# Kernel tuning notes

Measured on AMD Instinct MI355X. Metric: run time of the kernel, lower is better.

## Reference

```python
import jax, jax.numpy as jnp
import numpy as np
import math

# Model dims (see shape_source)
BATCH, SEQ, HH, WW = 32, 128, 32, 32   # x: (B, seq_len, H, W); L = H*W = 1024
D_MODEL = 1024                          # hidden_dim
N2 = 4                                  # n=8 -> 4 complex S4D modes
L_MAX = 64                              # SSM kernel length (l_max)


def _layernorm(x, gamma, beta, eps=1e-5):
    mu = jnp.mean(x, axis=-1, keepdims=True)
    var = jnp.var(x, axis=-1, keepdims=True)
    return (x - mu) * jax.lax.rsqrt(var + eps) * gamma + beta


def setup_inputs() -> dict:
    key = jax.random.key(0)
    ks = jax.random.split(key, 12)
    d_in = SEQ  # d_input = d_output = seq_len
    inp = {
        "x": jax.random.normal(ks[0], (BATCH, SEQ, HH, WW), dtype=jnp.float32),
        # encoder Linear(d_input -> d_model)
        "W_enc": jax.random.normal(ks[1], (d_in, D_MODEL), dtype=jnp.float32) / math.sqrt(d_in),
        "b_enc": jnp.zeros((D_MODEL,), dtype=jnp.float32),
        # S4D SSM parameters (per d_model channel, N2 complex modes)
        "log_dt": (jax.random.uniform(ks[2], (D_MODEL,), dtype=jnp.float32)
                   * (math.log(0.1) - math.log(0.001)) + math.log(0.001)),
        "A_log_real": jnp.full((D_MODEL, N2), math.log(0.5), dtype=jnp.float32),
        "A_imag": jnp.broadcast_to(math.pi * jnp.arange(N2, dtype=jnp.float32), (D_MODEL, N2)).copy(),
        "C_real": jax.random.normal(ks[3], (D_MODEL, N2), dtype=jnp.float32) * 0.5,
        "C_imag": jax.random.normal(ks[4], (D_MODEL, N2), dtype=jnp.float32) * 0.5,
        "D": jax.random.normal(ks[5], (D_MODEL,), dtype=jnp.float32),
        # position-wise GLU mixing Linear(d_model -> 2*d_model)
        "W_glu": jax.random.normal(ks[6], (D_MODEL, 2 * D_MODEL), dtype=jnp.float32) / math.sqrt(D_MODEL),
        "b_glu": jnp.zeros((2 * D_MODEL,), dtype=jnp.float32),
        "ln_gamma": jnp.ones((D_MODEL,), dtype=jnp.float32),
        "ln_beta": jnp.zeros((D_MODEL,), dtype=jnp.float32),
        # decoder Linear(d_model -> d_output)
        "W_dec": jax.random.normal(ks[7], (D_MODEL, d_in), dtype=jnp.float32) / math.sqrt(D_MODEL),
        "b_dec": jnp.zeros((d_in,), dtype=jnp.float32),
    }
    return inp


def reference(x, W_enc, b_enc, log_dt, A_log_real, A_imag, C_real, C_imag, D,
              W_glu, b_glu, ln_gamma, ln_beta, W_dec, b_dec):
    Bsz, S, Hh, Ww = x.shape
    L = Hh * Ww
    u = x.reshape(Bsz, S, L)                                  # (B, d_input, L)
    # encoder applied per position along L
    h = jnp.einsum('bdl,de->ble', u, W_enc) + b_enc           # (B, L, d_model)

    # ---- S4D kernel (ZOH discretization, B=1, diagonal A) ----
    dt = jnp.exp(log_dt)                                      # (d,)
    A = -jnp.exp(A_log_real) + 1j * A_imag                    # (d, n2) complex
    Cc = C_real + 1j * C_imag
    dtA = A * dt[:, None]                                     # (d, n2)
    Bd = (jnp.exp(dtA) - 1.0) / A                             # ZOH input matrix
    t = jnp.arange(L_MAX)
    vand = jnp.exp(dtA[:, :, None] * t)                       # (d, n2, l_max)
    K = 2.0 * jnp.einsum('dn,dnl->dl', Cc * Bd, vand).real    # (d, l_max)

    # ---- causal FFT convolution along L + skip D*u ----
    z = jnp.swapaxes(h, 1, 2)                                 # (B, d, L)
    n_fft = L + L_MAX
    y = jnp.fft.irfft(jnp.fft.rfft(z, n=n_fft) * jnp.fft.rfft(K, n=n_fft), n=n_fft)[..., :L]
    y = y + D[:, None] * z                                    # (B, d, L)

    # ---- block: GELU -> GLU mixing -> residual -> LayerNorm ----
    y = jax.nn.gelu(jnp.swapaxes(y, 1, 2))                    # (B, L, d)
    g = y @ W_glu + b_glu                                     # (B, L, 2d)
    g = g[..., :D_MODEL] * jax.nn.sigmoid(g[..., D_MODEL:])
    h = _layernorm(h + g, ln_gamma, ln_beta)                  # (B, L, d)

    out = h @ W_dec + b_dec                                   # (B, L, d_output)
    out = jnp.swapaxes(out, 1, 2).reshape(Bsz, S, Hh, Ww)
    return out
```

## Files before the change

kernel.cpp:

```cpp
#include <hip/hip_runtime.h>
#include <hip/hip_bf16.h>
#include <math.h>

#define B_ 32
#define S_ 128
#define L_ 1024
#define D_ 1024

typedef unsigned short u16;
typedef __attribute__((ext_vector_type(8))) __bf16 bf16x8;
typedef __attribute__((ext_vector_type(8))) short short8;
typedef __attribute__((ext_vector_type(4))) float f32x4;

__device__ __forceinline__ float bf2f(u16 u) {
    return __uint_as_float(((unsigned)u) << 16);
}
__device__ __forceinline__ u16 f2bf(float f) {
    unsigned u = __float_as_uint(f);
    u += 0x7FFF + ((u >> 16) & 1);
    return (u16)(u >> 16);
}
__device__ __forceinline__ float gelu_tanh(float x) {
    float x3 = x * x * x;
    float t = tanhf(0.7978845608028654f * (x + 0.044715f * x3));
    return 0.5f * x * (1.0f + t);
}
__device__ __forceinline__ float sigmoidf(float x) {
    return 1.0f / (1.0f + expf(-x));
}
__device__ __forceinline__ void gld16(const void* g, void* l) {
    __builtin_amdgcn_global_load_lds((const __attribute__((address_space(1))) void*)g,
                                     (__attribute__((address_space(3))) void*)l, 16, 0, 0);
}

__device__ __forceinline__ void tcast_body(
        const float* __restrict__ src, u16* __restrict__ dst, int R, int C,
        const float* __restrict__ rowscale, int bx, int by, int t,
        float (*tile)[65]) {
    int c0 = bx * 64, r0 = by * 64;
    #pragma unroll
    for (int p = 0; p < 4; ++p) {
        int fid = p * 256 + t;
        int rr = fid >> 4, cc = (fid & 15) * 4;
        float4 v = *(const float4*)&src[(size_t)(r0 + rr) * C + c0 + cc];
        float sc = rowscale ? rowscale[r0 + rr] : 1.0f;
        tile[rr][cc + 0] = v.x * sc; tile[rr][cc + 1] = v.y * sc;
        tile[rr][cc + 2] = v.z * sc; tile[rr][cc + 3] = v.w * sc;
    }
    __syncthreads();
    #pragma unroll
    for (int p = 0; p < 4; ++p) {
        int fid = p * 256 + t;
        int rr = fid >> 4, cc = (fid & 15) * 4;
        ushort4 o;
        o.x = f2bf(tile[cc + 0][rr]);
        o.y = f2bf(tile[cc + 1][rr]);
        o.z = f2bf(tile[cc + 2][rr]);
        o.w = f2bf(tile[cc + 3][rr]);
        *(ushort4*)&dst[(size_t)(c0 + rr) * R + r0 + cc] = o;
    }
}

__global__ __launch_bounds__(256) void k_prep(
        const float* __restrict__ Wg, u16* __restrict__ WgT,
        const float* __restrict__ Wd, const float* __restrict__ gam,
        u16* __restrict__ WdT,
        const float* __restrict__ We, u16* __restrict__ WeT,
        const float* __restrict__ x, u16* __restrict__ xb,
        const float* __restrict__ ldt, const float* __restrict__ Alr,
        const float* __restrict__ Aim, const float* __restrict__ Cr,
        const float* __restrict__ Ci, float* __restrict__ Kt,
        const float* __restrict__ bet, const float* __restrict__ bd,
        float* __restrict__ c12) {
    __shared__ float tile[64][65];
    __shared__ float r1[4], r2[4];
    int blk = blockIdx.x;
    int t = threadIdx.x;
    if (blk < 512) {
        tcast_body(Wg, WgT, 1024, 2048, nullptr, blk & 31, blk >> 5, t, tile);
    } else if (blk < 544) {
        int id = blk - 512;
        tcast_body(Wd, WdT, 1024, 128, gam, id & 1, id >> 1, t, tile);
    } else if (blk < 576) {
        int id = blk - 544;
        tcast_body(We, WeT, 128, 1024, nullptr, id & 15, id >> 4, t, tile);
    } else if (blk < 1600) {
        int id = blk - 576;
        int bz = id >> 5;
        tcast_body(x + (size_t)bz * 131072, xb + (size_t)bz * 131072,
                   128, 1024, nullptr, id & 15, (id >> 4) & 1, t, tile);
    } else if (blk < 1856) {
        int tid = (blk - 1600) * 256 + t;
        int d = tid & (D_ - 1);
        int j = tid >> 10;
        float dt = expf(ldt[d]);
        float acc = 0.f;
        #pragma unroll
        for (int n = 0; n < 4; ++n) {
            float ar = -expf(Alr[d * 4 + n]);
            float ai = Aim[d * 4 + n];
            float wr = ar * dt, wi = ai * dt;
            float ew = expf(wr);
            float sw, cw; sincosf(wi, &sw, &cw);
            float ur = ew * cw - 1.0f, ui = ew * sw;
            float inv = 1.0f / (ar * ar + ai * ai);
            float bdr = (ur * ar + ui * ai) * inv;
            float bdi = (ui * ar - ur * ai) * inv;
            float cr = Cr[d * 4 + n], ci = Ci[d * 4 + n];
            float cbr = cr * bdr - ci * bdi;
            float cbi = cr * bdi + ci * bdr;
            float ej = expf(wr * (float)j);
            float sj, cj; sincosf(wi * (float)j, &sj, &cj);
            acc += 2.0f * ej * (cbr * cj - cbi * sj);
        }
        Kt[j * D_ + d] = acc;
    } else {
        int s = blk - 1856;
        float a1 = 0.f, a2 = 0.f;
        #pragma unroll
        for (int it = 0; it < 4; ++it) {
            int k = it * 256 + t;
            float w = Wd[(size_t)k * 128 + s];
            a1 += gam[k] * w;
            a2 += bet[k] * w;
        }
        #pragma unroll
        for (int off = 32; off > 0; off >>= 1) {
            a1 += __shfl_down(a1, off);
            a2 += __shfl_down(a2, off);
        }
        int wid = t >> 6, lane = t & 63;
        if (lane == 0) { r1[wid] = a1; r2[wid] = a2; }
        __syncthreads();
        if (t == 0) {
            c12[s] = r1[0] + r1[1] + r1[2] + r1[3];
            c12[128 + s] = r2[0] + r2[1] + r2[2] + r2[3] + bd[s];
        }
    }
}

__global__ __launch_bounds__(256) void k_enc_mfma(
        const u16* __restrict__ xb, const u16* __restrict__ WeT,
        const float* __restrict__ be, u16* __restrict__ hb) {
    __shared__ u16 As[128 * 128];
    __shared__ u16 Bs[128 * 128];
    int t = threadIdx.x;
    int lane = t & 63, wid = t >> 6;
    int wr = wid & 1, wc = wid >> 1;
    int orig = blockIdx.x;
    int wgid = (orig & 7) * 256 + (orig >> 3);
    int m0 = (wgid >> 3) * 128;
    int e0 = (wgid & 7) * 128;

    #pragma unroll
    for (int c = 0; c < 8; ++c) {
        int ch = wid * 8 + c;
        int r = ch * 4 + (lane >> 4);
        int g = (lane & 15) ^ (r & 15);
        gld16(&xb[(size_t)(m0 + r) * 128 + g * 8], &As[ch * 512]);
        gld16(&WeT[(size_t)(e0 + r) * 128 + g * 8], &Bs[ch * 512]);
    }
    int co4[4];
    #pragma unroll
    for (int kh = 0; kh < 4; ++kh)
        co4[kh] = ((((lane >> 4) + kh * 4) ^ (lane & 15)) * 8);
    int arow[4], brow[4];
    #pragma unroll
    for (int i = 0; i < 4; ++i) arow[i] = (wr * 64 + i * 16 + (lane & 15)) * 128;
    #pragma unroll
    for (int q = 0; q < 4; ++q) brow[q] = (wc * 64 + q * 16 + (lane & 15)) * 128;

    __syncthreads();
    f32x4 acc[4][4] = {};
    #pragma unroll
    for (int kh = 0; kh < 4; ++kh) {
        bf16x8 af[4], bfr[4];
        #pragma unroll
        for (int i = 0; i < 4; ++i) af[i] = *(const bf16x8*)&As[arow[i] + co4[kh]];
        #pragma unroll
        for (int q = 0; q < 4; ++q) bfr[q] = *(const bf16x8*)&Bs[brow[q] + co4[kh]];
        __builtin_amdgcn_s_setprio(1);
        #pragma unroll
        for (int i = 0; i < 4; ++i)
            #pragma unroll
            for (int q = 0; q < 4; ++q)
                acc[i][q] = __builtin_amdgcn_mfma_f32_16x16x32_bf16(af[i], bfr[q], acc[i][q], 0, 0, 0);
        __builtin_amdgcn_s_setprio(0);
    }
    #pragma unroll
    for (int q = 0; q < 4; ++q) {
        int e = e0 + wc * 64 + q * 16 + (lane & 15);
        float bias = be[e];
        #pragma unroll
        for (int i = 0; i < 4; ++i) {
            #pragma unroll
            for (int r = 0; r < 4; ++r) {
                int m = m0 + wr * 64 + i * 16 + (lane >> 4) * 4 + r;
                hb[(size_t)m * 1024 + e] = f2bf(acc[i][q][r] + bias);
            }
        }
    }
}

__global__ __launch_bounds__(256) void k_conv(
        const u16* __restrict__ hb, const float* __restrict__ Kt,
        const float* __restrict__ Dv, u16* __restrict__ yg) {
    __shared__ float hs[128][68];
    int b = blockIdx.y;
    int d0 = blockIdx.x * 64;
    int t = threadIdx.x;
    int dl = t & 63, lg = t >> 6;
    {
        int r = 64 + (t >> 2), cg0 = (t & 3) * 16;
        #pragma unroll
        for (int j = 0; j < 4; ++j)
            *(float4*)&hs[r][cg0 + j * 4] = make_float4(0.f, 0.f, 0.f, 0.f);
    }
    float kr[64];
    #pragma unroll
    for (int j = 0; j < 64; ++j) kr[j] = Kt[j * 1024 + d0 + dl];
    float Dd = Dv[d0 + dl];
    int lr = t >> 2, cg = (t & 3) * 16;
    for (int it = 0; it < 16; ++it) {
        int l0 = it * 64;
        {
            int l = l0 + lr;
            int row = l & 127;
            const u16* src = &hb[((size_t)b * 1024 + l) * 1024 + d0 + cg];
            #pragma unroll
            for (int h = 0; h < 2; ++h) {
                ushort4 u0 = *(const ushort4*)&src[h * 8];
                ushort4 u1 = *(const ushort4*)&src[h * 8 + 4];
                *(float4*)&hs[row][cg + h * 8] =
                    make_float4(bf2f(u0.x), bf2f(u0.y), bf2f(u0.z), bf2f(u0.w));
                *(float4*)&hs[row][cg + h * 8 + 4] =
                    make_float4(bf2f(u1.x), bf2f(u1.y), bf2f(u1.z), bf2f(u1.w));
            }
        }
        __syncthreads();
        float acc[16] = {};
        int rb = l0 + 65 + lg * 16;
        #pragma unroll
        for (int s = 0; s < 15; ++s) {
            float hv = hs[(rb + s) & 127][dl];
            #pragma unroll
            for (int i = 0; i <= 14; ++i)
                if (i <= s) acc[i] = fmaf(kr[i + 63 - s], hv, acc[i]);
        }
        #pragma unroll
        for (int s = 15; s < 64; ++s) {
            float hv = hs[(rb + s) & 127][dl];
            #pragma unroll
            for (int i = 0; i < 16; ++i)
                acc[i] = fmaf(kr[i + 63 - s], hv, acc[i]);
        }
        #pragma unroll
        for (int s = 64; s < 79; ++s) {
            float hv = hs[(rb + s) & 127][dl];
            #pragma unroll
            for (int i = 1; i < 16; ++i)
                if (i >= s - 63) acc[i] = fmaf(kr[i + 63 - s], hv, acc[i]);
        }
        #pragma unroll
        for (int i = 0; i < 16; ++i) {
            int l = l0 + lg * 16 + i;
            float z = hs[l & 127][dl];
            float y = acc[i] + Dd * z;
            yg[((size_t)b * 1024 + l) * 1024 + d0 + dl] = f2bf(gelu_tanh(y));
        }
        __syncthreads();
    }
}

__global__ __launch_bounds__(512, 2) void k_glu256(
        const u16* __restrict__ yg, const u16* __restrict__ WgT,
        const float* __restrict__ bg, u16* __restrict__ hb) {
    __shared__ u16 S[65536];
    int t = threadIdx.x;
    int lane = t & 63, wid = t >> 6;
    int wr = wid >> 2, wc = wid & 3;

    int orig = blockIdx.x;
    int wgid = (orig & 7) * 128 + (orig >> 3);
    int m0 = (wgid >> 3) * 256;
    int p0g = (wgid & 7) * 128;

    int gofs = (((lane & 7) ^ ((lane >> 3) & 7)) * 8);
    int ch0 = wid * 2, ch1 = ch0 + 1;
    int dst0 = ch0 * 512 + lane * 8;
    int dst1 = ch1 * 512 + lane * 8;
    int gmA[2][2], gmB[2][2];
    #pragma unroll
    for (int h = 0; h < 2; ++h) {
        #pragma unroll
        for (int j = 0; j < 2; ++j) {
            int ch = ch0 + j;
            gmA[h][j] = m0 + (ch >> 3) * 128 + h * 64 + (ch & 7) * 8 + (lane >> 3);
            int r = (ch >> 2) * 64 + h * 32 + (ch & 3) * 8 + (lane >> 3);
            gmB[h][j] = ((r >> 4) & 1) * 1024 + p0g + (((r >> 5) << 4) | (r & 15));
        }
    }
    int co[2];
    co[0] = (((lane >> 4) + 0) ^ (lane & 7)) * 8;
    co[1] = (((lane >> 4) + 4) ^ (lane & 7)) * 8;
    int arow[4], brow[2];
    #pragma unroll
    for (int i = 0; i < 4; ++i) arow[i] = (wr * 64 + i * 16 + (lane & 15)) * 64;
    #pragma unroll
    for (int q = 0; q < 2; ++q) brow[q] = (wc * 32 + q * 16 + (lane & 15)) * 64;

#define GLD_A(H, BUF, K0) { u16* d_ = &S[((BUF) * 2 + (H)) * 8192]; \
    gld16(&yg[(size_t)gmA[H][0] * 1024 + (K0) + gofs], d_ + dst0); \
    gld16(&yg[(size_t)gmA[H][1] * 1024 + (K0) + gofs], d_ + dst1); }
#define GLD_B(H, BUF, K0) { u16* d_ = &S[32768 + ((BUF) * 2 + (H)) * 8192]; \
    gld16(&WgT[(size_t)gmB[H][0] * 1024 + (K0) + gofs], d_ + dst0); \
    gld16(&WgT[(size_t)gmB[H][1] * 1024 + (K0) + gofs], d_ + dst1); }

#define RD_AH(MS) { const u16* Ar_ = &S[(cbuf * 2 + (MS)) * 8192]; \
    _Pragma("unroll") for (int i = 0; i < 4; ++i) { \
        a_[i][0] = *(const bf16x8*)&Ar_[arow[i] + co[0]]; \
        a_[i][1] = *(const bf16x8*)&Ar_[arow[i] + co[1]]; } }
#define RD_BH(NS, BB) { const u16* Br_ = &S[32768 + (cbuf * 2 + (NS)) * 8192]; \
    _Pragma("unroll") for (int q = 0; q < 2; ++q) { \
        BB[q][0] = *(const bf16x8*)&Br_[brow[q] + co[0]]; \
        BB[q][1] = *(const bf16x8*)&Br_[brow[q] + co[1]]; } }
#define MFMA16(MS, NS, BB) { __builtin_amdgcn_s_setprio(1); \
    _Pragma("unroll") for (int i = 0; i < 4; ++i) \
        _Pragma("unroll") for (int q = 0; q < 2; ++q) { \
            acc[(MS) * 4 + i][(NS) * 2 + q] = __builtin_amdgcn_mfma_f32_16x16x32_bf16( \
                a_[i][0], BB[q][0], acc[(MS) * 4 + i][(NS) * 2 + q], 0, 0, 0); \
            acc[(MS) * 4 + i][(NS) * 2 + q] = __builtin_amdgcn_mfma_f32_16x16x32_bf16( \
                a_[i][1], BB[q][1], acc[(MS) * 4 + i][(NS) * 2 + q], 0, 0, 0); } \
    __builtin_amdgcn_s_setprio(0); }

    f32x4 acc[8][4] = {};
    bf16x8 a_[4][2], b0_[2][2], b1_[2][2];

    GLD_A(0, 0, 0); GLD_B(0, 0, 0); GLD_B(1, 0, 0); GLD_A(1, 0, 0);
    GLD_A(0, 1, 64); GLD_B(0, 1, 64);

    for (int kt = 0; kt < 15; ++kt) {
        int cbuf = kt & 1, nbuf = cbuf ^ 1;
        int k1 = (kt + 1) * 64, k2 = (kt + 2) * 64;
        asm volatile("s_waitcnt vmcnt(4)" ::: "memory");
        __builtin_amdgcn_s_barrier();
        __builtin_amdgcn_sched_barrier(0);
        RD_AH(0); RD_BH(0, b0_); RD_BH(1, b1_);
        GLD_B(1, nbuf, k1);
        GLD_A(1, nbuf, k1);
        MFMA16(0, 0, b0_);
        MFMA16(0, 1, b1_);
        RD_AH(1);
        __builtin_amdgcn_s_barrier();
        __builtin_amdgcn_sched_barrier(0);
        if (kt < 14) { GLD_A(0, cbuf, k2); GLD_B(0, cbuf, k2); }
        MFMA16(1, 0, b0_);
        MFMA16(1, 1, b1_);
    }
    {
        int cbuf = 1;
        asm volatile("s_waitcnt vmcnt(0)" ::: "memory");
        __builtin_amdgcn_s_barrier();
        __builtin_amdgcn_sched_barrier(0);
        RD_AH(0); RD_BH(0, b0_); RD_BH(1, b1_);
        MFMA16(0, 0, b0_);
        MFMA16(0, 1, b1_);
        RD_AH(1);
        MFMA16(1, 0, b0_);
        MFMA16(1, 1, b1_);
    }
#undef GLD_A
#undef GLD_B
#undef RD_AH
#undef RD_BH
#undef MFMA16

    #pragma unroll
    for (int i = 0; i < 8; ++i) {
        #pragma unroll
        for (int pb = 0; pb < 2; ++pb) {
            int col = p0g + (wc * 2 + pb) * 16 + (lane & 15);
            float b1v = bg[col];
            float b2v = bg[1024 + col];
            #pragma unroll
            for (int r = 0; r < 4; ++r) {
                int m = m0 + wr * 128 + i * 16 + (lane >> 4) * 4 + r;
                size_t idx = (size_t)m * 1024 + col;
                float g1 = acc[i][pb * 2][r] + b1v;
                float g2 = acc[i][pb * 2 + 1][r] + b2v;
                hb[idx] = f2bf(bf2f(hb[idx]) + g1 * sigmoidf(g2));
            }
        }
    }
}

__global__ __launch_bounds__(256) void k_dec_mfma(
        const u16* __restrict__ hb, const u16* __restrict__ WdT,
        const float* __restrict__ c12, float* __restrict__ out) {
    __shared__ __align__(16) char smem[66560];
    u16* As = (u16*)smem;
    u16* Bs = (u16*)(smem + 32768);
    float* Ts = (float*)smem;
    float* muL = (float*)(smem + 65536);
    float* rsL = (float*)(smem + 65536 + 512);
    int t = threadIdx.x;
    int lane = t & 63, wid = t >> 6;
    int wr = wid & 1, wc = wid >> 1;
    int m0 = blockIdx.x * 128;
    int bb = m0 >> 10, l0 = m0 & 1023;

    int gsrc = (((lane & 7) ^ (lane >> 3)) * 8);
    int rr4[4];
    #pragma unroll
    for (int c = 0; c < 4; ++c) rr4[c] = (wid * 4 + c) * 8 + (lane >> 3);
    int co[2];
    co[0] = (((lane >> 4) + 0) ^ (lane & 7)) * 8;
    co[1] = (((lane >> 4) + 4) ^ (lane & 7)) * 8;
    int arow[4], brow[4];
    #pragma unroll
    for (int i = 0; i < 4; ++i) arow[i] = (wr * 64 + i * 16 + (lane & 15)) * 64;
    #pragma unroll
    for (int q = 0; q < 4; ++q) brow[q] = (wc * 64 + q * 16 + (lane & 15)) * 64;

    f32x4 acc[4][4] = {};
    float s1[4] = {}, s2[4] = {};
    #pragma unroll
    for (int c = 0; c < 4; ++c) {
        int ch = wid * 4 + c;
        gld16(&hb[(size_t)(m0 + rr4[c]) * 1024 + gsrc], &As[0 * 8192 + ch * 512]);
        gld16(&WdT[(size_t)rr4[c] * 1024 + gsrc], &Bs[0 * 8192 + ch * 512]);
    }
    __syncthreads();
    int cur = 0;
    for (int kt = 0; kt < 16; ++kt) {
        if (kt < 15) {
            int k0 = (kt + 1) * 64;
            #pragma unroll
            for (int c = 0; c < 4; ++c) {
                int ch = wid * 4 + c;
                gld16(&hb[(size_t)(m0 + rr4[c]) * 1024 + k0 + gsrc], &As[(cur ^ 1) * 8192 + ch * 512]);
                gld16(&WdT[(size_t)rr4[c] * 1024 + k0 + gsrc], &Bs[(cur ^ 1) * 8192 + ch * 512]);
            }
        }
        #pragma unroll
        for (int kh = 0; kh < 2; ++kh) {
            bf16x8 af[4], bfr[4];
            #pragma unroll
            for (int i = 0; i < 4; ++i) af[i] = *(const bf16x8*)&As[cur * 8192 + arow[i] + co[kh]];
            #pragma unroll
            for (int q = 0; q < 4; ++q) bfr[q] = *(const bf16x8*)&Bs[cur * 8192 + brow[q] + co[kh]];
            if (wid < 2) {
                #pragma unroll
                for (int i = 0; i < 4; ++i) {
                    short8 sa = *(short8*)&af[i];
                    #pragma unroll
                    for (int e = 0; e < 8; ++e) {
                        float v = bf2f((u16)sa[e]);
                        s1[i] += v;
                        s2[i] = fmaf(v, v, s2[i]);
                    }
                }
            }
            __builtin_amdgcn_s_setprio(1);
            #pragma unroll
            for (int i = 0; i < 4; ++i)
                #pragma unroll
                for (int q = 0; q < 4; ++q)
                    acc[i][q] = __builtin_amdgcn_mfma_f32_16x16x32_bf16(af[i], bfr[q], acc[i][q], 0, 0, 0);
            __builtin_amdgcn_s_setprio(0);
        }
        __syncthreads();
        cur ^= 1;
    }
    if (wid < 2) {
        #pragma unroll
        for (int i = 0; i < 4; ++i) {
            s1[i] += __shfl_xor(s1[i], 16);
            s2[i] += __shfl_xor(s2[i], 16);
            s1[i] += __shfl_xor(s1[i], 32);
            s2[i] += __shfl_xor(s2[i], 32);
            if (lane < 16) {
                int ml = wr * 64 + i * 16 + lane;
                float mu = s1[i] * (1.0f / 1024.0f);
                float var = s2[i] * (1.0f / 1024.0f) - mu * mu;
                muL[ml] = mu;
                rsL[ml] = rsqrtf(var + 1e-5f);
            }
        }
    }
    __syncthreads();
    #pragma unroll
    for (int ro = 0; ro < 2; ++ro) {
        if (wc == ro) {
            #pragma unroll
            for (int i = 0; i < 4; ++i)
                #pragma unroll
                for (int q = 0; q < 4; ++q) {
                    int sl = q * 16 + (lane & 15);
                    float c1v = c12[ro * 64 + sl];
                    float c2v = c12[128 + ro * 64 + sl];
                    #pragma unroll
                    for (int r = 0; r < 4; ++r) {
                        int ml = wr * 64 + i * 16 + (lane >> 4) * 4 + r;
                        float rst = rsL[ml];
                        Ts[sl * 132 + ml] = rst * acc[i][q][r] - muL[ml] * rst * c1v + c2v;
                    }
                }
        }
        __syncthreads();
        #pragma unroll
        for (int p = 0; p < 8; ++p) {
            int fid = p * 256 + t;
            int sl = fid >> 5, c = (fid & 31) * 4;
            float4 v = *(const float4*)&Ts[sl * 132 + c];
            *(float4*)&out[(size_t)bb * 131072 + (size_t)(ro * 64 + sl) * 1024 + l0 + c] = v;
        }
        __syncthreads();
    }
}

extern "C" void kernel_launch(void* const* d_in, const int* in_sizes, int n_in,
                              void* d_out, int out_size, void* d_ws, size_t ws_size,
                              hipStream_t stream) {
    (void)in_sizes; (void)n_in; (void)out_size; (void)ws_size;
    const float* x   = (const float*)d_in[0];
    const float* We  = (const float*)d_in[1];
    const float* be  = (const float*)d_in[2];
    const float* ldt = (const float*)d_in[3];
    const float* Alr = (const float*)d_in[4];
    const float* Aim = (const float*)d_in[5];
    const float* Cr  = (const float*)d_in[6];
    const float* Ci  = (const float*)d_in[7];
    const float* Dv  = (const float*)d_in[8];
    const float* Wg  = (const float*)d_in[9];
    const float* bg  = (const float*)d_in[10];
    const float* gam = (const float*)d_in[11];
    const float* bet = (const float*)d_in[12];
    const float* Wd  = (const float*)d_in[13];
    const float* bd  = (const float*)d_in[14];
    float* out = (float*)d_out;

    u16* hb = (u16*)d_ws;
    u16* yg = hb + 33554432ull;
    float* Kt = (float*)(yg + 33554432ull);
    u16* WgT = (u16*)(Kt + 65536);
    u16* WdT = WgT + 2097152ull;
    u16* WeT = WdT + 131072ull;
    float* c12 = (float*)(WeT + 131072ull);
    u16* xb  = yg;

    k_prep<<<1984, 256, 0, stream>>>(Wg, WgT, Wd, gam, WdT, We, WeT, x, xb,
                                     ldt, Alr, Aim, Cr, Ci, Kt, bet, bd, c12);
    k_enc_mfma<<<2048, 256, 0, stream>>>(xb, WeT, be, hb);
    k_conv<<<dim3(16, 32), 256, 0, stream>>>(hb, Kt, Dv, yg);
    k_glu256<<<1024, 512, 0, stream>>>(yg, WgT, bg, hb);
    k_dec_mfma<<<256, 256, 0, stream>>>(hb, WdT, c12, out);
}
```

Baseline: 321.9 us.

## Split encoder GEMM K into two smem stages, stage output, prefetch conv rows

The encoder MFMA kernel now loads K in two 64-wide chunks, which halves the shared-memory tile so more blocks can be resident (launch bounds set to 4 blocks). Its output is staged through shared memory and written back to global memory as coalesced 16-byte stores instead of scattered 2-byte stores. The conv kernel software-prefetches the next tile of h into registers while the current tile is being computed, hiding global load latency. The costs are an extra barrier per K chunk in the encoder and extra registers in the conv kernel.

```diff
diff --git a/kernel.cpp b/kernel.cpp
--- a/kernel.cpp
+++ b/kernel.cpp
@@ -139,11 +139,12 @@
     }
 }
 
-__global__ __launch_bounds__(256) void k_enc_mfma(
+__global__ __launch_bounds__(256, 4) void k_enc_mfma(
         const u16* __restrict__ xb, const u16* __restrict__ WeT,
         const float* __restrict__ be, u16* __restrict__ hb) {
-    __shared__ u16 As[128 * 128];
-    __shared__ u16 Bs[128 * 128];
+    __shared__ __align__(16) u16 S[17408];
+    u16* As = S;
+    u16* Bs = S + 8192;
     int t = threadIdx.x;
     int lane = t & 63, wid = t >> 6;
     int wr = wid & 1, wc = wid >> 1;
@@ -152,53 +153,66 @@
     int m0 = (wgid >> 3) * 128;
     int e0 = (wgid & 7) * 128;
 
-    #pragma unroll
-    for (int c = 0; c < 8; ++c) {
-        int ch = wid * 8 + c;
-        int r = ch * 4 + (lane >> 4);
-        int g = (lane & 15) ^ (r & 15);
-        gld16(&xb[(size_t)(m0 + r) * 128 + g * 8], &As[ch * 512]);
-        gld16(&WeT[(size_t)(e0 + r) * 128 + g * 8], &Bs[ch * 512]);
-    }
-    int co4[4];
-    #pragma unroll
-    for (int kh = 0; kh < 4; ++kh)
-        co4[kh] = ((((lane >> 4) + kh * 4) ^ (lane & 15)) * 8);
+    int gofs = (((lane & 7) ^ ((lane >> 3) & 7)) * 8);
+    int rloc[4];
+    #pragma unroll
+    for (int c = 0; c < 4; ++c) rloc[c] = (wid * 4 + c) * 8 + (lane >> 3);
+    int co[2];
+    co[0] = (((lane >> 4) + 0) ^ (lane & 7)) * 8;
+    co[1] = (((lane >> 4) + 4) ^ (lane & 7)) * 8;
     int arow[4], brow[4];
     #pragma unroll
-    for (int i = 0; i < 4; ++i) arow[i] = (wr * 64 + i * 16 + (lane & 15)) * 128;
-    #pragma unroll
-    for (int q = 0; q < 4; ++q) brow[q] = (wc * 64 + q * 16 + (lane & 15)) * 128;
-
+    for (int i = 0; i < 4; ++i) arow[i] = (wr * 64 + i * 16 + (lane & 15)) * 64;
+    #pragma unroll
+    for (int q = 0; q < 4; ++q) brow[q] = (wc * 64 + q * 16 + (lane & 15)) * 64;
+
+    f32x4 acc[4][4] = {};
+    #pragma unroll
+    for (int kt = 0; kt < 2; ++kt) {
+        if (kt) __syncthreads();
+        int k0 = kt * 64;
+        #pragma unroll
+        for (int c = 0; c < 4; ++c) {
+            int ch = wid * 4 + c;
+            gld16(&xb[(size_t)(m0 + rloc[c]) * 128 + k0 + gofs], &As[ch * 512]);
+            gld16(&WeT[(size_t)(e0 + rloc[c]) * 128 + k0 + gofs], &Bs[ch * 512]);
+        }
+        __syncthreads();
+        #pragma unroll
+        for (int kh = 0; kh < 2; ++kh) {
+            bf16x8 af[4], bfr[4];
+            #pragma unroll
+            for (int i = 0; i < 4; ++i) af[i] = *(const bf16x8*)&As[arow[i] + co[kh]];
+            #pragma unroll
+            for (int q = 0; q < 4; ++q) bfr[q] = *(const bf16x8*)&Bs[brow[q] + co[kh]];
+            __builtin_amdgcn_s_setprio(1);
+            #pragma unroll
+            for (int i = 0; i < 4; ++i)
+                #pragma unroll
+                for (int q = 0; q < 4; ++q)
+                    acc[i][q] = __builtin_amdgcn_mfma_f32_16x16x32_bf16(af[i], bfr[q], acc[i][q], 0, 0, 0);
+            __builtin_amdgcn_s_setprio(0);
+        }
+    }
     __syncthreads();
-    f32x4 acc[4][4] = {};
-    #pragma unroll
-    for (int kh = 0; kh < 4; ++kh) {
-        bf16x8 af[4], bfr[4];
-        #pragma unroll
-        for (int i = 0; i < 4; ++i) af[i] = *(const bf16x8*)&As[arow[i] + co4[kh]];
-        #pragma unroll
-        for (int q = 0; q < 4; ++q) bfr[q] = *(const bf16x8*)&Bs[brow[q] + co4[kh]];
-        __builtin_amdgcn_s_setprio(1);
+    #pragma unroll
+    for (int q = 0; q < 4; ++q) {
+        int e = wc * 64 + q * 16 + (lane & 15);
+        float bias = be[e0 + e];
         #pragma unroll
         for (int i = 0; i < 4; ++i)
             #pragma unroll
-            for (int q = 0; q < 4; ++q)
-                acc[i][q] = __builtin_amdgcn_mfma_f32_16x16x32_bf16(af[i], bfr[q], acc[i][q], 0, 0, 0);
-        __builtin_amdgcn_s_setprio(0);
-    }
-    #pragma unroll
-    for (int q = 0; q < 4; ++q) {
-        int e = e0 + wc * 64 + q * 16 + (lane & 15);
-        float bias = be[e];
-        #pragma unroll
-        for (int i = 0; i < 4; ++i) {
-            #pragma unroll
             for (int r = 0; r < 4; ++r) {
-                int m = m0 + wr * 64 + i * 16 + (lane >> 4) * 4 + r;
-                hb[(size_t)m * 1024 + e] = f2bf(acc[i][q][r] + bias);
+                int m = wr * 64 + i * 16 + (lane >> 4) * 4 + r;
+                S[m * 136 + e] = f2bf(acc[i][q][r] + bias);
             }
-        }
+    }
+    __syncthreads();
+    #pragma unroll
+    for (int p = 0; p < 8; ++p) {
+        int fid = p * 256 + t;
+        int row = fid >> 4, cg = (fid & 15) * 8;
+        *(uint4*)&hb[(size_t)(m0 + row) * 1024 + e0 + cg] = *(const uint4*)&S[row * 136 + cg];
     }
 }
 
@@ -221,23 +235,23 @@
     for (int j = 0; j < 64; ++j) kr[j] = Kt[j * 1024 + d0 + dl];
     float Dd = Dv[d0 + dl];
     int lr = t >> 2, cg = (t & 3) * 16;
+    uint4 pref0, pref1;
+#define LOADP(IT) { const u16* src = &hb[((size_t)b * 1024 + (IT) * 64 + lr) * 1024 + d0 + cg]; \
+    pref0 = *(const uint4*)&src[0]; pref1 = *(const uint4*)&src[8]; }
+    LOADP(0);
     for (int it = 0; it < 16; ++it) {
         int l0 = it * 64;
         {
-            int l = l0 + lr;
-            int row = l & 127;
-            const u16* src = &hb[((size_t)b * 1024 + l) * 1024 + d0 + cg];
-            #pragma unroll
-            for (int h = 0; h < 2; ++h) {
-                ushort4 u0 = *(const ushort4*)&src[h * 8];
-                ushort4 u1 = *(const ushort4*)&src[h * 8 + 4];
-                *(float4*)&hs[row][cg + h * 8] =
-                    make_float4(bf2f(u0.x), bf2f(u0.y), bf2f(u0.z), bf2f(u0.w));
-                *(float4*)&hs[row][cg + h * 8 + 4] =
-                    make_float4(bf2f(u1.x), bf2f(u1.y), bf2f(u1.z), bf2f(u1.w));
-            }
-        }
-        __syncthreads();
+            int row = (l0 + lr) & 127;
+            const u16* pu0 = (const u16*)&pref0;
+            const u16* pu1 = (const u16*)&pref1;
+            #pragma unroll
+            for (int e = 0; e < 8; ++e) hs[row][cg + e] = bf2f(pu0[e]);
+            #pragma unroll
+            for (int e = 0; e < 8; ++e) hs[row][cg + 8 + e] = bf2f(pu1[e]);
+        }
+        __syncthreads();
+        if (it < 15) LOADP(it + 1);
         float acc[16] = {};
         int rb = l0 + 65 + lg * 16;
         #pragma unroll
@@ -270,6 +284,7 @@
         }
         __syncthreads();
     }
+#undef LOADP
 }
 
 __global__ __launch_bounds__(512, 2) void k_glu256(
```

Measured after the change: 323.9 us, median of 2. Within noise of the previous version (+0.6%).
